# Performance work log

Hardware: AMD Instinct MI355X
Metric: run time of the kernel (lower is better)

## Reference

```python
import jax, jax.numpy as jnp
import numpy as np

B, S, D = 32, 4096, 512

def setup_inputs() -> dict:
    key = jax.random.key(0)
    ks = jax.random.split(key, 5)
    scale = 1.0 / np.sqrt(D)
    return {
        "query": jax.random.normal(ks[0], (B, D), jnp.float32),
        "values": jax.random.normal(ks[1], (B, S, D), jnp.float32),
        "W1": jax.random.normal(ks[2], (D, D), jnp.float32) * scale,
        "b1": jnp.zeros((D,), jnp.float32),
        "W2": jax.random.normal(ks[3], (D, D), jnp.float32) * scale,
        "b2": jnp.zeros((D,), jnp.float32),
        "V": jax.random.normal(ks[4], (D, 1), jnp.float32) * scale,
        "bv": jnp.zeros((1,), jnp.float32),
    }

def reference(query, values, W1, b1, W2, b2, V, bv):
    # query: [B, D], values: [B, S, D]
    q_proj = query @ W1 + b1                      # [B, D]
    v_proj = jnp.einsum('bsd,de->bse', values, W2) + b2  # [B, S, D]
    hidden = jnp.tanh(q_proj[:, None, :] + v_proj)       # [B, S, D]
    score = jnp.einsum('bsd,de->bse', hidden, V) + bv    # [B, S, 1]
    attn = jax.nn.softmax(score, axis=1)                 # softmax over seq axis
    context = jnp.sum(attn * values, axis=1)             # [B, D]
    return (context, attn)
```

## Files before the change

### kernel.cpp

```cpp
#include <hip/hip_runtime.h>
#include <hip/hip_bf16.h>
#include <stdint.h>

#define NB 32
#define NS 4096
#define ND 512

typedef __attribute__((ext_vector_type(8))) short short8;
typedef __attribute__((ext_vector_type(4))) float floatx4;
typedef __attribute__((ext_vector_type(4))) unsigned int uint4v;

__device__ __forceinline__ short f2bf(float f) {
    unsigned int u = __builtin_bit_cast(unsigned int, f);
    return (short)((u + 0x8000u) >> 16);
}

__device__ __forceinline__ unsigned int cvt_pk_bf16(float lo, float hi) {
    unsigned int r;
    asm("v_cvt_pk_bf16_f32 %0, %1, %2" : "=v"(r) : "v"(lo), "v"(hi));
    return r;
}

__device__ __forceinline__ float fast_tanh(float x) {
    float e = __expf(2.0f * x);
    return 1.0f - 2.0f * __builtin_amdgcn_rcpf(e + 1.0f);
}

__global__ void __launch_bounds__(256) qproj_kernel(
    const float* __restrict__ query, const float* __restrict__ W1,
    const float* __restrict__ b1, const float* __restrict__ b2,
    float* __restrict__ qb) {
    const int b  = blockIdx.x;
    const int es = blockIdx.y;
    const int t  = threadIdx.x;
    const int col = t & 63, kc = t >> 6;
    __shared__ float q[ND];
    __shared__ float red[256];
    q[t] = query[b * ND + t];
    q[t + 256] = query[b * ND + t + 256];
    __syncthreads();
    float acc = 0.f;
    const float* wp = W1 + (size_t)(kc * 128) * ND + es * 64 + col;
    const float* qp = q + kc * 128;
#pragma unroll 8
    for (int k = 0; k < 128; k++)
        acc += qp[k] * wp[(size_t)k * ND];
    red[t] = acc;
    __syncthreads();
    if (t < 64) {
        float s = red[t] + red[t + 64] + red[t + 128] + red[t + 192];
        int e = es * 64 + t;
        qb[b * ND + e] = s + b1[e] + b2[e];
    }
}

__global__ void __launch_bounds__(256) w2t_kernel(
    const float* __restrict__ W2, unsigned short* __restrict__ W2Tt) {
    int g = blockIdx.x * 256 + threadIdx.x;
    int nt = g >> 14;
    int ks = (g >> 10) & 15;
    int kq = (g >> 8) & 3;
    int n  = g & 255;
    int e  = nt * 256 + n;
    int k0 = ks * 32 + kq * 8;
    short8 v;
#pragma unroll
    for (int j = 0; j < 8; j++)
        v[j] = f2bf(W2[(size_t)(k0 + j) * ND + e]);
    *(short8*)&W2Tt[(size_t)g * 8] = v;
}

__global__ void __launch_bounds__(256, 3) scores_kernel(
    const float* __restrict__ values, const unsigned short* __restrict__ W2Tt,
    const float* __restrict__ qb, const float* __restrict__ V,
    float* __restrict__ pscores) {
    const int nt = blockIdx.x;
    const int st = blockIdx.y;
    const int b  = blockIdx.z;
    const int n0 = nt * 256, s0 = st * 64;

    __shared__ __align__(16) unsigned short sA[2][2048];
    __shared__ float sQb[256];
    __shared__ float sV[256];
    __shared__ float sRed[4][64];

    const int tid  = threadIdx.x;
    const int lane = tid & 63;
    const int wave = tid >> 6;
    const int mr = lane & 15;
    const int q  = lane >> 4;

    sQb[tid] = qb[b * ND + n0 + tid];
    sV[tid]  = V[n0 + tid];

    floatx4 acc[4][4] = {};

    const int arow = tid >> 2;
    const int ac   = tid & 3;
    const int ardo = arow * 32 + ((ac ^ ((tid >> 3) & 3)) * 8);
    const float* ag = values + ((size_t)b * NS + s0 + arow) * ND + ac * 8;

    const int afo = (q ^ ((mr >> 1) & 3)) * 8;

    const unsigned short* bp = W2Tt + (size_t)nt * 16 * 8192 + (q * 256 + wave * 64 + mr) * 8;

    float4 p0 = *(const float4*)(ag);
    float4 p1 = *(const float4*)(ag + 4);
    float4 aq[3][2];
    aq[1][0] = *(const float4*)(ag + 32);  aq[1][1] = *(const float4*)(ag + 36);
    aq[2][0] = *(const float4*)(ag + 64);  aq[2][1] = *(const float4*)(ag + 68);
    short8 bq[2][4];
#pragma unroll
    for (int j = 0; j < 4; j++)
        bq[0][j] = *(const short8*)(bp + j * 128);
    {
        uint4v w;
        w.x = cvt_pk_bf16(p0.x, p0.y); w.y = cvt_pk_bf16(p0.z, p0.w);
        w.z = cvt_pk_bf16(p1.x, p1.y); w.w = cvt_pk_bf16(p1.z, p1.w);
        *(uint4v*)&sA[0][ardo] = w;
    }
    asm volatile("s_waitcnt lgkmcnt(0)" ::: "memory");
    __builtin_amdgcn_s_barrier();
    __builtin_amdgcn_sched_barrier(0);

#pragma unroll
    for (int ks = 0; ks < 16; ks++) {
        const int cur = ks & 1, nxt = cur ^ 1;

        short8 af[4];
#pragma unroll
        for (int i = 0; i < 4; i++)
            af[i] = *(const short8*)&sA[cur][(i * 16 + mr) * 32 + afo];

        if (ks < 15) {
            const float4 a0 = aq[(ks + 1) % 3][0], a1 = aq[(ks + 1) % 3][1];
            uint4v w;
            w.x = cvt_pk_bf16(a0.x, a0.y); w.y = cvt_pk_bf16(a0.z, a0.w);
            w.z = cvt_pk_bf16(a1.x, a1.y); w.w = cvt_pk_bf16(a1.z, a1.w);
            *(uint4v*)&sA[nxt][ardo] = w;
        }

        if (ks < 15) {
            const unsigned short* bsrc = bp + (size_t)(ks + 1) * 8192;
#pragma unroll
            for (int j = 0; j < 4; j++)
                bq[nxt][j] = *(const short8*)(bsrc + j * 128);
        }
        if (ks < 13) {
            aq[ks % 3][0] = *(const float4*)(ag + (ks + 3) * 32);
            aq[ks % 3][1] = *(const float4*)(ag + (ks + 3) * 32 + 4);
        }

        __builtin_amdgcn_s_setprio(1);
#pragma unroll
        for (int i = 0; i < 4; i++)
#pragma unroll
            for (int j = 0; j < 4; j++)
                acc[i][j] = __builtin_amdgcn_mfma_f32_16x16x32_bf16(af[i], bq[cur][j], acc[i][j], 0, 0, 0);
        __builtin_amdgcn_s_setprio(0);

        asm volatile("s_waitcnt lgkmcnt(0)" ::: "memory");
        __builtin_amdgcn_s_barrier();
        __builtin_amdgcn_sched_barrier(0);
    }

    float vcoef[4], qadd[4];
#pragma unroll
    for (int j = 0; j < 4; j++) {
        int col = wave * 64 + j * 16 + mr;
        vcoef[j] = sV[col];
        qadd[j]  = sQb[col];
    }

#pragma unroll
    for (int i = 0; i < 4; i++) {
#pragma unroll
        for (int r = 0; r < 4; r++) {
            float p = 0.f;
#pragma unroll
            for (int j = 0; j < 4; j++)
                p += fast_tanh(acc[i][j][r] + qadd[j]) * vcoef[j];
            p += __shfl_xor(p, 1);
            p += __shfl_xor(p, 2);
            p += __shfl_xor(p, 4);
            p += __shfl_xor(p, 8);
            if (mr == 0) sRed[wave][i * 16 + q * 4 + r] = p;
        }
    }
    __syncthreads();
    if (tid < 64) {
        float s = sRed[0][tid] + sRed[1][tid] + sRed[2][tid] + sRed[3][tid];
        pscores[((size_t)nt * NB + b) * NS + s0 + tid] = s;
    }
}

__global__ void __launch_bounds__(256) softmax_kernel(
    const float* __restrict__ pscores, float* __restrict__ attn) {
    int b = blockIdx.x;
    int t = threadIdx.x;
    __shared__ float red[4];
    __shared__ float bcast[2];
    const float* sc0 = pscores + (size_t)b * NS;
    const float* sc1 = pscores + (size_t)(NB + b) * NS;
    float v[16];
    float m = -1e30f;
#pragma unroll
    for (int i = 0; i < 16; i++) {
        v[i] = sc0[t + i * 256] + sc1[t + i * 256];
        m = fmaxf(m, v[i]);
    }
    for (int o = 32; o; o >>= 1) m = fmaxf(m, __shfl_xor(m, o));
    if ((t & 63) == 0) red[t >> 6] = m;
    __syncthreads();
    if (t == 0) bcast[0] = fmaxf(fmaxf(red[0], red[1]), fmaxf(red[2], red[3]));
    __syncthreads();
    m = bcast[0];
    float sum = 0.f;
#pragma unroll
    for (int i = 0; i < 16; i++) { v[i] = __expf(v[i] - m); sum += v[i]; }
    for (int o = 32; o; o >>= 1) sum += __shfl_xor(sum, o);
    if ((t & 63) == 0) red[t >> 6] = sum;
    __syncthreads();
    if (t == 0) bcast[1] = red[0] + red[1] + red[2] + red[3];
    __syncthreads();
    float inv = 1.0f / bcast[1];
    float* ao = attn + (size_t)b * NS;
#pragma unroll
    for (int i = 0; i < 16; i++) ao[t + i * 256] = v[i] * inv;
}

__global__ void __launch_bounds__(256) context_partial_kernel(
    const float* __restrict__ values, const float* __restrict__ attn,
    float* __restrict__ pctx) {
    int sc = blockIdx.x;
    int b  = blockIdx.y;
    int t  = threadIdx.x;
    __shared__ float sAttn[256];
    __shared__ float4 sRed4[256];
    sAttn[t] = attn[(size_t)b * NS + sc * 256 + t];
    __syncthreads();
    const int half = t >> 7;
    const int d0 = (t & 127) * 4;
    const float* vp = values + ((size_t)b * NS + sc * 256 + half) * ND + d0;
    float4 acc = {0.f, 0.f, 0.f, 0.f};
#pragma unroll 8
    for (int s = 0; s < 128; s++) {
        float a = sAttn[s * 2 + half];
        float4 v = *(const float4*)(vp + (size_t)s * 2 * ND);
        acc.x += a * v.x; acc.y += a * v.y; acc.z += a * v.z; acc.w += a * v.w;
    }
    sRed4[t] = acc;
    __syncthreads();
    if (t < 128) {
        float4 r0 = sRed4[t], r1 = sRed4[t + 128];
        float4 o = {r0.x + r1.x, r0.y + r1.y, r0.z + r1.z, r0.w + r1.w};
        *(float4*)&pctx[((size_t)sc * 32 + b) * ND + d0] = o;
    }
}

__global__ void __launch_bounds__(256) context_reduce_kernel(
    const float* __restrict__ pctx, float* __restrict__ ctx) {
    int i = blockIdx.x * 256 + threadIdx.x;
    float s = 0.f;
#pragma unroll
    for (int p = 0; p < 16; p++) s += pctx[(size_t)p * (32 * ND) + i];
    ctx[i] = s;
}

extern "C" void kernel_launch(void* const* d_in, const int* in_sizes, int n_in,
                              void* d_out, int out_size, void* d_ws, size_t ws_size,
                              hipStream_t stream) {
    const float* query  = (const float*)d_in[0];
    const float* values = (const float*)d_in[1];
    const float* W1     = (const float*)d_in[2];
    const float* b1     = (const float*)d_in[3];
    const float* W2     = (const float*)d_in[4];
    const float* b2     = (const float*)d_in[5];
    const float* V      = (const float*)d_in[6];

    float* ctx_out  = (float*)d_out;
    float* attn_out = (float*)d_out + NB * ND;

    char* ws = (char*)d_ws;
    float*          qb      = (float*)ws;
    unsigned short* W2Tt    = (unsigned short*)(ws + (64 << 10));
    float*          pscores = (float*)(ws + (576 << 10));
    float*          pctx    = pscores;

    qproj_kernel<<<dim3(NB, 8), 256, 0, stream>>>(query, W1, b1, b2, qb);
    w2t_kernel<<<128, 256, 0, stream>>>(W2, W2Tt);
    scores_kernel<<<dim3(2, 64, 32), 256, 0, stream>>>(values, W2Tt, qb, V, pscores);
    softmax_kernel<<<NB, 256, 0, stream>>>(pscores, attn_out);
    context_partial_kernel<<<dim3(16, 32), 256, 0, stream>>>(values, attn_out, pctx);
    context_reduce_kernel<<<64, 256, 0, stream>>>(pctx, ctx_out);
}
```

Measured before the change: 465.7 us.

## Deepen scores prefetch pipeline and split context partial over more blocks

The scores kernel now triple-buffers W2 fragments, prefetching two k-steps ahead, and keeps four stages of values rows in flight. Scheduling barriers pin the order of the loads relative to the MFMA block. The context partial kernel splits the sequence into 32 chunks of 128 instead of 16 chunks of 256, and each thread handles two columns without an LDS reduction. This gives more blocks for parallelism, at the cost of a larger partial buffer that now sits in its own workspace region and a reduction over 32 partials. The deeper prefetch raises register use, which may lower occupancy.

```diff
diff --git a/kernel.cpp b/kernel.cpp
--- a/kernel.cpp
+++ b/kernel.cpp
@@ -106,13 +106,17 @@
 
     float4 p0 = *(const float4*)(ag);
     float4 p1 = *(const float4*)(ag + 4);
-    float4 aq[3][2];
+    short8 bq[3][4];
+#pragma unroll
+    for (int j = 0; j < 4; j++)
+        bq[0][j] = *(const short8*)(bp + j * 128);
+#pragma unroll
+    for (int j = 0; j < 4; j++)
+        bq[1][j] = *(const short8*)(bp + 8192 + j * 128);
+    float4 aq[4][2];
     aq[1][0] = *(const float4*)(ag + 32);  aq[1][1] = *(const float4*)(ag + 36);
     aq[2][0] = *(const float4*)(ag + 64);  aq[2][1] = *(const float4*)(ag + 68);
-    short8 bq[2][4];
-#pragma unroll
-    for (int j = 0; j < 4; j++)
-        bq[0][j] = *(const short8*)(bp + j * 128);
+    aq[3][0] = *(const float4*)(ag + 96);  aq[3][1] = *(const float4*)(ag + 100);
     {
         uint4v w;
         w.x = cvt_pk_bf16(p0.x, p0.y); w.y = cvt_pk_bf16(p0.z, p0.w);
@@ -133,30 +137,33 @@
             af[i] = *(const short8*)&sA[cur][(i * 16 + mr) * 32 + afo];
 
         if (ks < 15) {
-            const float4 a0 = aq[(ks + 1) % 3][0], a1 = aq[(ks + 1) % 3][1];
+            const float4 a0 = aq[(ks + 1) & 3][0], a1 = aq[(ks + 1) & 3][1];
             uint4v w;
             w.x = cvt_pk_bf16(a0.x, a0.y); w.y = cvt_pk_bf16(a0.z, a0.w);
             w.z = cvt_pk_bf16(a1.x, a1.y); w.w = cvt_pk_bf16(a1.z, a1.w);
             *(uint4v*)&sA[nxt][ardo] = w;
         }
-
-        if (ks < 15) {
-            const unsigned short* bsrc = bp + (size_t)(ks + 1) * 8192;
+        __builtin_amdgcn_sched_barrier(0);
+
+        if (ks < 14) {
+            const unsigned short* bsrc = bp + (size_t)(ks + 2) * 8192;
 #pragma unroll
             for (int j = 0; j < 4; j++)
-                bq[nxt][j] = *(const short8*)(bsrc + j * 128);
-        }
-        if (ks < 13) {
-            aq[ks % 3][0] = *(const float4*)(ag + (ks + 3) * 32);
-            aq[ks % 3][1] = *(const float4*)(ag + (ks + 3) * 32 + 4);
-        }
+                bq[(ks + 2) % 3][j] = *(const short8*)(bsrc + j * 128);
+        }
+        __builtin_amdgcn_sched_barrier(0);
+        if (ks < 12) {
+            aq[(ks + 4) & 3][0] = *(const float4*)(ag + (ks + 4) * 32);
+            aq[(ks + 4) & 3][1] = *(const float4*)(ag + (ks + 4) * 32 + 4);
+        }
+        __builtin_amdgcn_sched_barrier(0);
 
         __builtin_amdgcn_s_setprio(1);
 #pragma unroll
         for (int i = 0; i < 4; i++)
 #pragma unroll
             for (int j = 0; j < 4; j++)
-                acc[i][j] = __builtin_amdgcn_mfma_f32_16x16x32_bf16(af[i], bq[cur][j], acc[i][j], 0, 0, 0);
+                acc[i][j] = __builtin_amdgcn_mfma_f32_16x16x32_bf16(af[i], bq[ks % 3][j], acc[i][j], 0, 0, 0);
         __builtin_amdgcn_s_setprio(0);
 
         asm volatile("s_waitcnt lgkmcnt(0)" ::: "memory");
@@ -235,27 +242,20 @@
     int sc = blockIdx.x;
     int b  = blockIdx.y;
     int t  = threadIdx.x;
-    __shared__ float sAttn[256];
-    __shared__ float4 sRed4[256];
-    sAttn[t] = attn[(size_t)b * NS + sc * 256 + t];
-    __syncthreads();
-    const int half = t >> 7;
-    const int d0 = (t & 127) * 4;
-    const float* vp = values + ((size_t)b * NS + sc * 256 + half) * ND + d0;
-    float4 acc = {0.f, 0.f, 0.f, 0.f};
+    __shared__ float sAttn[128];
+    if (t < 128) sAttn[t] = attn[(size_t)b * NS + sc * 128 + t];
+    __syncthreads();
+    int d = t * 2;
+    const float2* vp = (const float2*)(values + ((size_t)b * NS + sc * 128) * ND + d);
+    float ax = 0.f, ay = 0.f;
 #pragma unroll 8
     for (int s = 0; s < 128; s++) {
-        float a = sAttn[s * 2 + half];
-        float4 v = *(const float4*)(vp + (size_t)s * 2 * ND);
-        acc.x += a * v.x; acc.y += a * v.y; acc.z += a * v.z; acc.w += a * v.w;
-    }
-    sRed4[t] = acc;
-    __syncthreads();
-    if (t < 128) {
-        float4 r0 = sRed4[t], r1 = sRed4[t + 128];
-        float4 o = {r0.x + r1.x, r0.y + r1.y, r0.z + r1.z, r0.w + r1.w};
-        *(float4*)&pctx[((size_t)sc * 32 + b) * ND + d0] = o;
-    }
+        float a = sAttn[s];
+        float2 v = vp[(size_t)s * 256];
+        ax += a * v.x; ay += a * v.y;
+    }
+    pctx[((size_t)sc * 32 + b) * ND + d]     = ax;
+    pctx[((size_t)sc * 32 + b) * ND + d + 1] = ay;
 }
 
 __global__ void __launch_bounds__(256) context_reduce_kernel(
@@ -263,7 +263,7 @@
     int i = blockIdx.x * 256 + threadIdx.x;
     float s = 0.f;
 #pragma unroll
-    for (int p = 0; p < 16; p++) s += pctx[(size_t)p * (32 * ND) + i];
+    for (int p = 0; p < 32; p++) s += pctx[(size_t)p * (32 * ND) + i];
     ctx[i] = s;
 }
 
@@ -285,12 +285,12 @@
     float*          qb      = (float*)ws;
     unsigned short* W2Tt    = (unsigned short*)(ws + (64 << 10));
     float*          pscores = (float*)(ws + (576 << 10));
-    float*          pctx    = pscores;
+    float*          pctx    = (float*)(ws + (1600 << 10));
 
     qproj_kernel<<<dim3(NB, 8), 256, 0, stream>>>(query, W1, b1, b2, qb);
     w2t_kernel<<<128, 256, 0, stream>>>(W2, W2Tt);
     scores_kernel<<<dim3(2, 64, 32), 256, 0, stream>>>(values, W2Tt, qb, V, pscores);
     softmax_kernel<<<NB, 256, 0, stream>>>(pscores, attn_out);
-    context_partial_kernel<<<dim3(16, 32), 256, 0, stream>>>(values, attn_out, pctx);
+    context_partial_kernel<<<dim3(32, 32), 256, 0, stream>>>(values, attn_out, pctx);
     context_reduce_kernel<<<64, 256, 0, stream>>>(pctx, ctx_out);
 }
```

Measured after the change: 469.9 us. No clear change (+0.9%).
